# Kernel optimization log

Measured on AMD Instinct MI355X. Metric: run time of the kernel, lower is better.

## Reference

```python
import jax, jax.numpy as jnp
import numpy as np

C = 256      # d_model
H = 8        # nhead
DF = 1024    # dim_feedforward
LE = 2048    # ego tokens
LA = 2048    # other-agent tokens
N_MATCH = 1024


def setup_inputs() -> dict:
    key = jax.random.key(0)
    ks = jax.random.split(key, 16)
    def rn(k, shape, s=0.02):
        return jax.random.normal(k, shape, dtype=jnp.float32) * s
    inp = {}
    inp['x_ego'] = jax.random.normal(ks[0], (LE, C), dtype=jnp.float32)
    inp['x_agent'] = jax.random.normal(ks[1], (LA, C), dtype=jnp.float32)
    # query_fusion MLP(2C -> C -> C -> C), torch Linear weight is (out, in)
    inp['Wf1'] = rn(ks[2], (C, 2 * C)); inp['bf1'] = jnp.zeros((C,), jnp.float32)
    inp['Wf2'] = rn(ks[3], (C, C));     inp['bf2'] = jnp.zeros((C,), jnp.float32)
    inp['Wf3'] = rn(ks[4], (C, C));     inp['bf3'] = jnp.zeros((C,), jnp.float32)
    # nn.MultiheadAttention packed in-proj and out-proj
    inp['Wqkv'] = rn(ks[5], (3 * C, C)); inp['bqkv'] = jnp.zeros((3 * C,), jnp.float32)
    inp['Wo'] = rn(ks[6], (C, C));       inp['bo'] = jnp.zeros((C,), jnp.float32)
    # FFN
    inp['W1'] = rn(ks[7], (DF, C)); inp['b1'] = jnp.zeros((DF,), jnp.float32)
    inp['W2'] = rn(ks[8], (C, DF)); inp['b2'] = jnp.zeros((C,), jnp.float32)
    # LayerNorms
    inp['g1'] = jnp.ones((C,), jnp.float32); inp['be1'] = jnp.zeros((C,), jnp.float32)
    inp['g2'] = jnp.ones((C,), jnp.float32); inp['be2'] = jnp.zeros((C,), jnp.float32)
    # unique 1D positions: first N_MATCH agent positions overlap ego, rest don't
    inp['pos_ego'] = jnp.arange(LE, dtype=jnp.int32)
    pa = np.concatenate([np.arange(N_MATCH), np.arange(LA - N_MATCH) + 10_000_000])
    inp['pos_agent'] = jnp.asarray(pa, dtype=jnp.int32)
    inp['n_remain'] = LA - N_MATCH  # static python int
    return inp


def _ln(t, g, b):
    m = t.mean(-1, keepdims=True)
    v = t.var(-1, keepdims=True)
    return (t - m) / jnp.sqrt(v + 1e-5) * g + b


def reference(x_ego, x_agent, Wf1, bf1, Wf2, bf2, Wf3, bf3, Wqkv, bqkv, Wo, bo,
              W1, b1, W2, b2, g1, be1, g2, be2, pos_ego, pos_agent, n_remain):
    # ---- position-keyed grouping / fuse (replaces the host-side dict loop) ----
    eq = pos_agent[:, None] == pos_ego[None, :]          # [La, Le]
    matched_e = eq.any(axis=0)                           # ego token has same-pos agent token
    agent_for_ego = jnp.argmax(eq, axis=0)               # [Le] matching agent index (valid where matched)
    fused_in = jnp.concatenate([x_ego, x_agent[agent_for_ego]], axis=-1)  # [Le, 2C]
    h = jax.nn.relu(fused_in @ Wf1.T + bf1)
    h = jax.nn.relu(h @ Wf2.T + bf2)
    fused = h @ Wf3.T + bf3                              # query_fusion MLP output [Le, C]
    ego_out = jnp.where(matched_e[:, None], fused, x_ego)
    # agent tokens with no ego match, in original agent order (fixed count n_remain)
    remain_idx = jnp.nonzero(~eq.any(axis=1), size=n_remain)[0]
    q = jnp.concatenate([ego_out, x_agent[remain_idx]], axis=0)[None]  # (1, Lq, C)
    kv = jnp.concatenate([x_ego, x_agent], axis=0)[None]               # (1, Lk, C)
    # ---- MultiheadAttention (batch_first, eval: dropout off) ----
    Wq, Wk, Wv = jnp.split(Wqkv, 3, axis=0)
    bq, bk, bv = jnp.split(bqkv, 3, axis=0)
    dh = C // H
    def heads(t, W, b):
        return (t @ W.T + b).reshape(1, -1, H, dh).transpose(0, 2, 1, 3)
    qh, kh, vh = heads(q, Wq, bq), heads(kv, Wk, bk), heads(kv, Wv, bv)
    scores = jnp.einsum('bhqd,bhkd->bhqk', qh, kh) / (float(dh) ** 0.5)
    attn = jax.nn.softmax(scores, axis=-1)
    o = jnp.einsum('bhqk,bhkd->bhqd', attn, vh).transpose(0, 2, 1, 3).reshape(1, -1, C)
    o = o @ Wo.T + bo
    # ---- residual + norm1 + FFN + residual + norm2 ----
    yq = _ln(q + o, g1, be1)
    ff = jax.nn.relu(yq @ W1.T + b1) @ W2.T + b2
    return _ln(yq + ff, g2, be2)
```

## Files before the change

kernel.cpp:

```cpp
#include <hip/hip_runtime.h>


#define LE 2048
#define LA 2048
#define CDIM 256
#define HN 8
#define DH 32
#define DFF 1024
#define NREM 1024
#define LQC 3072
#define LKC 4096
#define KSPLIT 4
#define NIT (LKC / KSPLIT / 64)

typedef unsigned short u16;
typedef unsigned int u32;
typedef __attribute__((ext_vector_type(8))) short bf16x8;
typedef __attribute__((ext_vector_type(4))) float f32x4;

__device__ __forceinline__ u32 pk_bf16(float a, float b) {
    u32 ua = (__builtin_bit_cast(u32, a) + 0x8000u) >> 16;
    u32 ub = (__builtin_bit_cast(u32, b) + 0x8000u) >> 16;
    return ua | (ub << 16);
}
__device__ __forceinline__ u16 bf16_1(float a) {
    return (u16)((__builtin_bit_cast(u32, a) + 0x8000u) >> 16);
}
__device__ __forceinline__ float fast_exp2(float x) {
    return __builtin_amdgcn_exp2f(x);
}
__device__ __forceinline__ bf16x8 pk8(const float* p) {
    float4 f0 = *(const float4*)p;
    float4 f1 = *(const float4*)(p + 4);
    union { u32 u[4]; bf16x8 v; } r;
    r.u[0] = pk_bf16(f0.x, f0.y); r.u[1] = pk_bf16(f0.z, f0.w);
    r.u[2] = pk_bf16(f1.x, f1.y); r.u[3] = pk_bf16(f1.z, f1.w);
    return r.v;
}

__global__ __launch_bounds__(1024) void k_match(const int* __restrict__ pos_ego,
                                                const int* __restrict__ pos_agent,
                                                int* __restrict__ afe,
                                                int* __restrict__ matched,
                                                int* __restrict__ remain) {
    __shared__ int keyA[4096], valA[4096], keyE[4096];
    __shared__ int ssum[1024];
    const int t = threadIdx.x;
#pragma unroll
    for (int i = 0; i < 4; ++i) { keyA[t + i * 1024] = -1; keyE[t + i * 1024] = -1; }
    __syncthreads();
#pragma unroll
    for (int i = 0; i < 2; ++i) {
        int a = t + i * 1024;
        int p = pos_agent[a];
        u32 h = ((u32)p * 2654435761u) >> 20;
        while (true) {
            int prev = atomicCAS(&keyA[h], -1, p);
            if (prev == -1) { valA[h] = a; break; }
            h = (h + 1) & 4095;
        }
        int pe = pos_ego[a];
        u32 he = ((u32)pe * 2654435761u) >> 20;
        while (true) {
            int prev = atomicCAS(&keyE[he], -1, pe);
            if (prev == -1) break;
            he = (he + 1) & 4095;
        }
    }
    __syncthreads();
#pragma unroll
    for (int i = 0; i < 2; ++i) {
        int e = t + i * 1024;
        int p = pos_ego[e];
        u32 h = ((u32)p * 2654435761u) >> 20;
        int idx = 0, fnd = 0;
        while (true) {
            int k = keyA[h];
            if (k == p) { idx = valA[h]; fnd = 1; break; }
            if (k == -1) break;
            h = (h + 1) & 4095;
        }
        afe[e] = idx;
        matched[e] = fnd;
    }
    int f[2];
#pragma unroll
    for (int i = 0; i < 2; ++i) {
        int a = t * 2 + i;
        int p = pos_agent[a];
        u32 h = ((u32)p * 2654435761u) >> 20;
        int fnd = 0;
        while (true) {
            int k = keyE[h];
            if (k == p) { fnd = 1; break; }
            if (k == -1) break;
            h = (h + 1) & 4095;
        }
        f[i] = !fnd;
    }
    int cnt = f[0] + f[1];
    ssum[t] = cnt;
    __syncthreads();
    for (int off = 1; off < 1024; off <<= 1) {
        int v = (t >= off) ? ssum[t - off] : 0;
        __syncthreads();
        ssum[t] += v;
        __syncthreads();
    }
    int pos = ssum[t] - cnt;
    if (f[0]) { if (pos < NREM) remain[pos] = t * 2; pos++; }
    if (f[1]) { if (pos < NREM) remain[pos] = t * 2 + 1; }
}

template <int EPI, bool RELU>
__global__ __launch_bounds__(256) void gemm_bw(const u16* __restrict__ A,
                                               const float* __restrict__ B,
                                               const float* __restrict__ bias,
                                               void* __restrict__ C,
                                               int M, int N, int K) {
    const int tid = threadIdx.x;
    const int w = tid >> 6, lane = tid & 63;
    const int quad = lane >> 4, qi = lane & 15;
    const int wm = w >> 1, wn = w & 1;
    const int bm = blockIdx.y * 64, bn = blockIdx.x * 64;

    const u16* pa0 = A + (size_t)(bm + wm * 32 + qi) * K + quad * 8;
    const u16* pa1 = pa0 + (size_t)16 * K;
    const float* pb0 = B + (size_t)(bn + wn * 32 + qi) * K + quad * 8;
    const float* pb1 = pb0 + (size_t)16 * K;

    f32x4 acc00 = {0.f, 0.f, 0.f, 0.f}, acc01 = {0.f, 0.f, 0.f, 0.f};
    f32x4 acc10 = {0.f, 0.f, 0.f, 0.f}, acc11 = {0.f, 0.f, 0.f, 0.f};

#pragma unroll 4
    for (int k = 0; k < K; k += 32) {
        bf16x8 a0 = *(const bf16x8*)(pa0 + k);
        bf16x8 a1 = *(const bf16x8*)(pa1 + k);
        bf16x8 b0 = pk8(pb0 + k);
        bf16x8 b1 = pk8(pb1 + k);
        acc00 = __builtin_amdgcn_mfma_f32_16x16x32_bf16(a0, b0, acc00, 0, 0, 0);
        acc01 = __builtin_amdgcn_mfma_f32_16x16x32_bf16(a0, b1, acc01, 0, 0, 0);
        acc10 = __builtin_amdgcn_mfma_f32_16x16x32_bf16(a1, b0, acc10, 0, 0, 0);
        acc11 = __builtin_amdgcn_mfma_f32_16x16x32_bf16(a1, b1, acc11, 0, 0, 0);
    }

#pragma unroll
    for (int i = 0; i < 2; ++i) {
#pragma unroll
        for (int j = 0; j < 2; ++j) {
            f32x4 acc = (i == 0) ? (j == 0 ? acc00 : acc01) : (j == 0 ? acc10 : acc11);
            int n = bn + wn * 32 + j * 16 + qi;
            int mbase = bm + wm * 32 + i * 16 + quad * 4;
            float bs = bias[n];
#pragma unroll
            for (int r = 0; r < 4; ++r) {
                float x = acc[r] + bs;
                if (RELU) x = fmaxf(x, 0.f);
                if (EPI == 0) ((float*)C)[(size_t)(mbase + r) * N + n] = x;
                else ((u16*)C)[(size_t)(mbase + r) * N + n] = bf16_1(x);
            }
        }
    }
}

__global__ __launch_bounds__(256) void k_mlp1(const float* __restrict__ x_ego,
                                              const float* __restrict__ x_agent,
                                              const int* __restrict__ afe,
                                              const float* __restrict__ Wf1,
                                              const float* __restrict__ bf1,
                                              u16* __restrict__ h1_b) {
    const int tid = threadIdx.x;
    const int w = tid >> 6, lane = tid & 63;
    const int quad = lane >> 4, qi = lane & 15;
    const int wm = w >> 1, wn = w & 1;
    const int bm = blockIdx.y * 64, bn = blockIdx.x * 64;

    int e0 = bm + wm * 32 + qi, e1 = e0 + 16;
    const float* pe0 = x_ego + (size_t)e0 * CDIM + quad * 8;
    const float* pe1 = x_ego + (size_t)e1 * CDIM + quad * 8;
    const float* pg0 = x_agent + (size_t)afe[e0] * CDIM + quad * 8;
    const float* pg1 = x_agent + (size_t)afe[e1] * CDIM + quad * 8;
    const float* pb0 = Wf1 + (size_t)(bn + wn * 32 + qi) * 512 + quad * 8;
    const float* pb1 = pb0 + (size_t)16 * 512;

    f32x4 acc00 = {0.f, 0.f, 0.f, 0.f}, acc01 = {0.f, 0.f, 0.f, 0.f};
    f32x4 acc10 = {0.f, 0.f, 0.f, 0.f}, acc11 = {0.f, 0.f, 0.f, 0.f};

#pragma unroll 4
    for (int k = 0; k < 256; k += 32) {
        bf16x8 a0 = pk8(pe0 + k);
        bf16x8 a1 = pk8(pe1 + k);
        bf16x8 b0 = pk8(pb0 + k);
        bf16x8 b1 = pk8(pb1 + k);
        acc00 = __builtin_amdgcn_mfma_f32_16x16x32_bf16(a0, b0, acc00, 0, 0, 0);
        acc01 = __builtin_amdgcn_mfma_f32_16x16x32_bf16(a0, b1, acc01, 0, 0, 0);
        acc10 = __builtin_amdgcn_mfma_f32_16x16x32_bf16(a1, b0, acc10, 0, 0, 0);
        acc11 = __builtin_amdgcn_mfma_f32_16x16x32_bf16(a1, b1, acc11, 0, 0, 0);
    }
#pragma unroll 4
    for (int k = 0; k < 256; k += 32) {
        bf16x8 a0 = pk8(pg0 + k);
        bf16x8 a1 = pk8(pg1 + k);
        bf16x8 b0 = pk8(pb0 + 256 + k);
        bf16x8 b1 = pk8(pb1 + 256 + k);
        acc00 = __builtin_amdgcn_mfma_f32_16x16x32_bf16(a0, b0, acc00, 0, 0, 0);
        acc01 = __builtin_amdgcn_mfma_f32_16x16x32_bf16(a0, b1, acc01, 0, 0, 0);
        acc10 = __builtin_amdgcn_mfma_f32_16x16x32_bf16(a1, b0, acc10, 0, 0, 0);
        acc11 = __builtin_amdgcn_mfma_f32_16x16x32_bf16(a1, b1, acc11, 0, 0, 0);
    }

#pragma unroll
    for (int i = 0; i < 2; ++i) {
#pragma unroll
        for (int j = 0; j < 2; ++j) {
            f32x4 acc = (i == 0) ? (j == 0 ? acc00 : acc01) : (j == 0 ? acc10 : acc11);
            int n = bn + wn * 32 + j * 16 + qi;
            int mbase = bm + wm * 32 + i * 16 + quad * 4;
            float bs = bf1[n];
#pragma unroll
            for (int r = 0; r < 4; ++r)
                h1_b[(size_t)(mbase + r) * 256 + n] = bf16_1(fmaxf(acc[r] + bs, 0.f));
        }
    }
}

__global__ __launch_bounds__(256) void k_mlp3f(const u16* __restrict__ h2_b,
                                               const float* __restrict__ Wf3,
                                               const float* __restrict__ bf3,
                                               const int* __restrict__ matched,
                                               const int* __restrict__ remain,
                                               const float* __restrict__ x_ego,
                                               const float* __restrict__ x_agent,
                                               float* __restrict__ qbuf,
                                               u16* __restrict__ qbuf_b) {
    const int tid = threadIdx.x;
    const int bm = blockIdx.y * 64, bn = blockIdx.x * 64;
    if (bm >= LE) {
        int row = bm + (tid >> 2);
        int col = bn + (tid & 3) * 16;
        int idx = remain[row - LE];
        idx = min(max(idx, 0), LA - 1);
        const float* src = x_agent + (size_t)idx * CDIM + col;
        float* dq = qbuf + (size_t)row * CDIM + col;
        u16* db = qbuf_b + (size_t)row * CDIM + col;
#pragma unroll
        for (int i = 0; i < 4; ++i) {
            float4 v = *(const float4*)(src + i * 4);
            *(float4*)(dq + i * 4) = v;
            u32 p0 = pk_bf16(v.x, v.y), p1 = pk_bf16(v.z, v.w);
            *(uint2*)(db + i * 4) = make_uint2(p0, p1);
        }
        return;
    }
    const int w = tid >> 6, lane = tid & 63;
    const int quad = lane >> 4, qi = lane & 15;
    const int wm = w >> 1, wn = w & 1;

    const u16* pa0 = h2_b + (size_t)(bm + wm * 32 + qi) * 256 + quad * 8;
    const u16* pa1 = pa0 + (size_t)16 * 256;
    const float* pb0 = Wf3 + (size_t)(bn + wn * 32 + qi) * 256 + quad * 8;
    const float* pb1 = pb0 + (size_t)16 * 256;

    f32x4 acc00 = {0.f, 0.f, 0.f, 0.f}, acc01 = {0.f, 0.f, 0.f, 0.f};
    f32x4 acc10 = {0.f, 0.f, 0.f, 0.f}, acc11 = {0.f, 0.f, 0.f, 0.f};
#pragma unroll 4
    for (int k = 0; k < 256; k += 32) {
        bf16x8 a0 = *(const bf16x8*)(pa0 + k);
        bf16x8 a1 = *(const bf16x8*)(pa1 + k);
        bf16x8 b0 = pk8(pb0 + k);
        bf16x8 b1 = pk8(pb1 + k);
        acc00 = __builtin_amdgcn_mfma_f32_16x16x32_bf16(a0, b0, acc00, 0, 0, 0);
        acc01 = __builtin_amdgcn_mfma_f32_16x16x32_bf16(a0, b1, acc01, 0, 0, 0);
        acc10 = __builtin_amdgcn_mfma_f32_16x16x32_bf16(a1, b0, acc10, 0, 0, 0);
        acc11 = __builtin_amdgcn_mfma_f32_16x16x32_bf16(a1, b1, acc11, 0, 0, 0);
    }
#pragma unroll
    for (int i = 0; i < 2; ++i) {
#pragma unroll
        for (int j = 0; j < 2; ++j) {
            f32x4 acc = (i == 0) ? (j == 0 ? acc00 : acc01) : (j == 0 ? acc10 : acc11);
            int n = bn + wn * 32 + j * 16 + qi;
            int mbase = bm + wm * 32 + i * 16 + quad * 4;
            float bs = bf3[n];
#pragma unroll
            for (int r = 0; r < 4; ++r) {
                int row = mbase + r;
                float v = acc[r] + bs;
                if (!matched[row]) v = x_ego[(size_t)row * CDIM + n];
                qbuf[(size_t)row * CDIM + n] = v;
                qbuf_b[(size_t)row * CDIM + n] = bf16_1(v);
            }
        }
    }
}

__global__ __launch_bounds__(256) void k_qkv(const u16* __restrict__ qbuf_b,
                                             const float* __restrict__ x_ego,
                                             const float* __restrict__ x_agent,
                                             const float* __restrict__ Wqkv,
                                             const float* __restrict__ bqkv,
                                             u16* __restrict__ qb,
                                             u16* __restrict__ kbp,
                                             u16* __restrict__ vtb,
                                             float qscale) {
    int b = blockIdx.x;
    const int tid = threadIdx.x;
    const int w = tid >> 6, lane = tid & 63;
    const int quad = lane >> 4, qi = lane & 15;
    const int wm = w >> 1, wn = w & 1;

    f32x4 acc00 = {0.f, 0.f, 0.f, 0.f}, acc01 = {0.f, 0.f, 0.f, 0.f};
    f32x4 acc10 = {0.f, 0.f, 0.f, 0.f}, acc11 = {0.f, 0.f, 0.f, 0.f};

    if (b < 192) {
        const int bm = (b >> 2) * 64, bn = (b & 3) * 64;
        const u16* pa0 = qbuf_b + (size_t)(bm + wm * 32 + qi) * 256 + quad * 8;
        const u16* pa1 = pa0 + (size_t)16 * 256;
        const float* pb0 = Wqkv + (size_t)(bn + wn * 32 + qi) * 256 + quad * 8;
        const float* pb1 = pb0 + (size_t)16 * 256;
#pragma unroll 4
        for (int k = 0; k < 256; k += 32) {
            bf16x8 a0 = *(const bf16x8*)(pa0 + k);
            bf16x8 a1 = *(const bf16x8*)(pa1 + k);
            bf16x8 b0 = pk8(pb0 + k);
            bf16x8 b1 = pk8(pb1 + k);
            acc00 = __builtin_amdgcn_mfma_f32_16x16x32_bf16(a0, b0, acc00, 0, 0, 0);
            acc01 = __builtin_amdgcn_mfma_f32_16x16x32_bf16(a0, b1, acc01, 0, 0, 0);
            acc10 = __builtin_amdgcn_mfma_f32_16x16x32_bf16(a1, b0, acc10, 0, 0, 0);
            acc11 = __builtin_amdgcn_mfma_f32_16x16x32_bf16(a1, b1, acc11, 0, 0, 0);
        }
#pragma unroll
        for (int i = 0; i < 2; ++i)
#pragma unroll
            for (int j = 0; j < 2; ++j) {
                f32x4 acc = (i == 0) ? (j == 0 ? acc00 : acc01) : (j == 0 ? acc10 : acc11);
                int n = bn + wn * 32 + j * 16 + qi;
                int mbase = bm + wm * 32 + i * 16 + quad * 4;
                float bs = bqkv[n];
#pragma unroll
                for (int r = 0; r < 4; ++r)
                    qb[(size_t)(mbase + r) * 256 + n] = bf16_1((acc[r] + bs) * qscale);
            }
    } else {
        int c = b - 192;
        const int bm = (c >> 3) * 64, bn = (c & 7) * 64;
        int j0 = bm + wm * 32 + qi, j1 = j0 + 16;
        const float* base = (bm < LE) ? x_ego : (x_agent - (size_t)LE * CDIM);
        const float* pa0 = base + (size_t)j0 * CDIM + quad * 8;
        const float* pa1 = base + (size_t)j1 * CDIM + quad * 8;
        const float* pb0 = Wqkv + (size_t)(256 + bn + wn * 32 + qi) * 256 + quad * 8;
        const float* pb1 = pb0 + (size_t)16 * 256;
#pragma unroll 4
        for (int k = 0; k < 256; k += 32) {
            bf16x8 a0 = pk8(pa0 + k);
            bf16x8 a1 = pk8(pa1 + k);
            bf16x8 b0 = pk8(pb0 + k);
            bf16x8 b1 = pk8(pb1 + k);
            acc00 = __builtin_amdgcn_mfma_f32_16x16x32_bf16(a0, b0, acc00, 0, 0, 0);
            acc01 = __builtin_amdgcn_mfma_f32_16x16x32_bf16(a0, b1, acc01, 0, 0, 0);
            acc10 = __builtin_amdgcn_mfma_f32_16x16x32_bf16(a1, b0, acc10, 0, 0, 0);
            acc11 = __builtin_amdgcn_mfma_f32_16x16x32_bf16(a1, b1, acc11, 0, 0, 0);
        }
#pragma unroll
        for (int i = 0; i < 2; ++i)
#pragma unroll
            for (int j = 0; j < 2; ++j) {
                f32x4 acc = (i == 0) ? (j == 0 ? acc00 : acc01) : (j == 0 ? acc10 : acc11);
                int n = bn + wn * 32 + j * 16 + qi;
                int mbase = bm + wm * 32 + i * 16 + quad * 4;
                float bs = bqkv[256 + n];
                float v[4];
#pragma unroll
                for (int r = 0; r < 4; ++r) v[r] = acc[r] + bs;
                if (n < 256) {
#pragma unroll
                    for (int r = 0; r < 4; ++r)
                        kbp[(size_t)(mbase + r) * 256 + n] = bf16_1(v[r]);
                } else {
                    ushort4 o4;
                    o4.x = bf16_1(v[0]); o4.y = bf16_1(v[1]);
                    o4.z = bf16_1(v[2]); o4.w = bf16_1(v[3]);
                    *(ushort4*)(vtb + (size_t)(n - 256) * LKC + mbase) = o4;
                }
            }
    }
}

__global__ __launch_bounds__(256) void attn_mfma(const u16* __restrict__ qb,
                                                 const u16* __restrict__ kb,
                                                 const u16* __restrict__ vtb,
                                                 float* __restrict__ Pl,
                                                 float* __restrict__ Pacc) {
    __shared__ u16 Kt[2][64 * 32];
    __shared__ u16 Vt[2][32 * 64];
    __shared__ u16 plds[4][16 * 64];
    const int tid = threadIdx.x;
    const int w = tid >> 6, lane = tid & 63;
    const int quad = lane >> 4, qi = lane & 15;
    const int h = blockIdx.y, ks = blockIdx.z;
    const int q0 = blockIdx.x * 64 + w * 16;

    bf16x8 qf = *(const bf16x8*)(qb + (size_t)(q0 + qi) * CDIM + h * DH + quad * 8);

    f32x4 O0 = {0.f, 0.f, 0.f, 0.f}, O1 = {0.f, 0.f, 0.f, 0.f};
    float lsum = 0.f;

    const int krow = w * 16 + (lane >> 2), kcp = lane & 3;
    const int kc = kcp ^ (krow & 3);
    const u16* kg0 = kb + (size_t)krow * CDIM + h * DH + kc * 8;
    const int kdst = krow * 32 + kcp * 8;
    const int vd = w * 8 + (lane >> 3), vcp = lane & 7;
    const int vc = vcp ^ (vd & 7);
    const u16* vg0 = vtb + (size_t)(h * DH + vd) * LKC + vc * 8;
    const int vdst = vd * 64 + vcp * 8;

    const int ka0 = qi * 32 + ((quad ^ (qi & 3)) << 3);
    const int v00o = qi * 64 + ((quad ^ (qi & 7)) << 3);
    const int v01o = qi * 64 + (((quad + 4) ^ (qi & 7)) << 3);
    const int swz = (qi & 7);
    const int rd0 = qi * 64 + ((quad ^ swz) << 3);
    const int rd1 = qi * 64 + (((4 + quad) ^ swz) << 3);
    const int half = (quad & 1) << 2;

    int kt = ks * (LKC / KSPLIT);
    {
        bf16x8 kr = *(const bf16x8*)(kg0 + (size_t)kt * CDIM);
        bf16x8 vr = *(const bf16x8*)(vg0 + kt);
        *(bf16x8*)&Kt[0][kdst] = kr;
        *(bf16x8*)&Vt[0][vdst] = vr;
    }
    int buf = 0;
    for (int it = 0; it < NIT; ++it, kt += 64) {
        __syncthreads();
        bf16x8 knext, vnext;
        const bool more = (it + 1 < NIT);
        if (more) {
            knext = *(const bf16x8*)(kg0 + (size_t)(kt + 64) * CDIM);
            vnext = *(const bf16x8*)(vg0 + kt + 64);
        }

        bf16x8 a0 = *(const bf16x8*)&Kt[buf][ka0];
        bf16x8 a1 = *(const bf16x8*)&Kt[buf][ka0 + 16 * 32];
        bf16x8 a2 = *(const bf16x8*)&Kt[buf][ka0 + 32 * 32];
        bf16x8 a3 = *(const bf16x8*)&Kt[buf][ka0 + 48 * 32];
        f32x4 z = {0.f, 0.f, 0.f, 0.f};
        f32x4 s0 = __builtin_amdgcn_mfma_f32_16x16x32_bf16(a0, qf, z, 0, 0, 0);
        f32x4 s1 = __builtin_amdgcn_mfma_f32_16x16x32_bf16(a1, qf, z, 0, 0, 0);
        f32x4 s2 = __builtin_amdgcn_mfma_f32_16x16x32_bf16(a2, qf, z, 0, 0, 0);
        f32x4 s3 = __builtin_amdgcn_mfma_f32_16x16x32_bf16(a3, qf, z, 0, 0, 0);

        float p0[4], p1[4], p2[4], p3[4];
#pragma unroll
        for (int r = 0; r < 4; ++r) {
            p0[r] = fast_exp2(s0[r]); p1[r] = fast_exp2(s1[r]);
            p2[r] = fast_exp2(s2[r]); p3[r] = fast_exp2(s3[r]);
            lsum += p0[r] + p1[r] + p2[r] + p3[r];
        }

        u16* pb = &plds[w][0];
#pragma unroll
        for (int t = 0; t < 4; ++t) {
            int jg = t * 2 + (quad >> 1);
            int off = qi * 64 + ((jg ^ swz) << 3) + half;
            uint2 pw;
            float* pp = (t == 0) ? p0 : (t == 1) ? p1 : (t == 2) ? p2 : p3;
            pw.x = pk_bf16(pp[0], pp[1]);
            pw.y = pk_bf16(pp[2], pp[3]);
            *(uint2*)&pb[off] = pw;
        }
        bf16x8 pa0 = *(bf16x8*)&pb[rd0];
        bf16x8 pa1 = *(bf16x8*)&pb[rd1];

        bf16x8 v00 = *(const bf16x8*)&Vt[buf][v00o];
        bf16x8 v01 = *(const bf16x8*)&Vt[buf][v01o];
        bf16x8 v10 = *(const bf16x8*)&Vt[buf][v00o + 16 * 64];
        bf16x8 v11 = *(const bf16x8*)&Vt[buf][v01o + 16 * 64];
        O0 = __builtin_amdgcn_mfma_f32_16x16x32_bf16(pa0, v00, O0, 0, 0, 0);
        O0 = __builtin_amdgcn_mfma_f32_16x16x32_bf16(pa1, v01, O0, 0, 0, 0);
        O1 = __builtin_amdgcn_mfma_f32_16x16x32_bf16(pa0, v10, O1, 0, 0, 0);
        O1 = __builtin_amdgcn_mfma_f32_16x16x32_bf16(pa1, v11, O1, 0, 0, 0);

        if (more) {
            *(bf16x8*)&Kt[buf ^ 1][kdst] = knext;
            *(bf16x8*)&Vt[buf ^ 1][vdst] = vnext;
        }
        buf ^= 1;
    }

    lsum += __shfl_xor(lsum, 16, 64);
    lsum += __shfl_xor(lsum, 32, 64);

    int pbase = (h * KSPLIT + ks) * LQC + q0;
    if (quad == 0) Pl[pbase + qi] = lsum;
#pragma unroll
    for (int r = 0; r < 4; ++r) {
        int q = quad * 4 + r;
        float* pa = Pacc + (size_t)(pbase + q) * 32;
        pa[qi] = O0[r];
        pa[16 + qi] = O1[r];
    }
}

__global__ __launch_bounds__(256) void attn_combine(const float* __restrict__ Pl,
                                                    const float* __restrict__ Pacc,
                                                    u16* __restrict__ attn_b) {
    int t = blockIdx.x * 256 + threadIdx.x;
    int row = t >> 6;
    int h = (t >> 3) & 7;
    int d4 = t & 7;
    float L = 0.f;
    float o[4] = {};
#pragma unroll
    for (int ck = 0; ck < KSPLIT; ++ck) {
        size_t pidx = (size_t)(h * KSPLIT + ck) * LQC + row;
        L += Pl[pidx];
        float4 a = *(const float4*)(Pacc + pidx * 32 + d4 * 4);
        o[0] += a.x; o[1] += a.y; o[2] += a.z; o[3] += a.w;
    }
    float inv = 1.0f / L;
    ushort4 ov;
    ov.x = bf16_1(o[0] * inv); ov.y = bf16_1(o[1] * inv);
    ov.z = bf16_1(o[2] * inv); ov.w = bf16_1(o[3] * inv);
    *(ushort4*)(attn_b + (size_t)row * CDIM + h * DH + d4 * 4) = ov;
}

template <bool EMIT_BF16>
__global__ __launch_bounds__(256) void ln_kernel(const float* __restrict__ X,
                                                 const float* __restrict__ R,
                                                 const float* __restrict__ g,
                                                 const float* __restrict__ b,
                                                 float* __restrict__ out,
                                                 u16* __restrict__ out_b) {
    int lane = threadIdx.x & 63;
    int row = blockIdx.x * 4 + (threadIdx.x >> 6);
    const float* x = X + (size_t)row * CDIM;
    const float* r = R + (size_t)row * CDIM;
    float4 xv = *(const float4*)(x + lane * 4);
    float4 rv = *(const float4*)(r + lane * 4);
    float v[4] = {xv.x + rv.x, xv.y + rv.y, xv.z + rv.z, xv.w + rv.w};
    float s = v[0] + v[1] + v[2] + v[3];
    float sq = v[0] * v[0] + v[1] * v[1] + v[2] * v[2] + v[3] * v[3];
#pragma unroll
    for (int off = 32; off >= 1; off >>= 1) {
        s += __shfl_xor(s, off, 64);
        sq += __shfl_xor(sq, off, 64);
    }
    float mean = s * (1.f / 256.f);
    float var = sq * (1.f / 256.f) - mean * mean;
    float rstd = rsqrtf(var + 1e-5f);
    float4 gv = *(const float4*)(g + lane * 4);
    float4 bv = *(const float4*)(b + lane * 4);
    float4 o = make_float4((v[0] - mean) * rstd * gv.x + bv.x,
                           (v[1] - mean) * rstd * gv.y + bv.y,
                           (v[2] - mean) * rstd * gv.z + bv.z,
                           (v[3] - mean) * rstd * gv.w + bv.w);
    *(float4*)(out + (size_t)row * CDIM + lane * 4) = o;
    if (EMIT_BF16) {
        uint2 ob;
        ob.x = pk_bf16(o.x, o.y);
        ob.y = pk_bf16(o.z, o.w);
        *(uint2*)(out_b + (size_t)row * CDIM + lane * 4) = ob;
    }
}

extern "C" void kernel_launch(void* const* d_in, const int* in_sizes, int n_in,
                              void* d_out, int out_size, void* d_ws, size_t ws_size,
                              hipStream_t stream) {
    const float* x_ego = (const float*)d_in[0];
    const float* x_agent = (const float*)d_in[1];
    const float* Wf1 = (const float*)d_in[2];
    const float* bf1 = (const float*)d_in[3];
    const float* Wf2 = (const float*)d_in[4];
    const float* bf2 = (const float*)d_in[5];
    const float* Wf3 = (const float*)d_in[6];
    const float* bf3 = (const float*)d_in[7];
    const float* Wqkv = (const float*)d_in[8];
    const float* bqkv = (const float*)d_in[9];
    const float* Wo = (const float*)d_in[10];
    const float* bo = (const float*)d_in[11];
    const float* W1 = (const float*)d_in[12];
    const float* b1 = (const float*)d_in[13];
    const float* W2 = (const float*)d_in[14];
    const float* b2 = (const float*)d_in[15];
    const float* g1 = (const float*)d_in[16];
    const float* be1 = (const float*)d_in[17];
    const float* g2 = (const float*)d_in[18];
    const float* be2 = (const float*)d_in[19];
    const int* pos_ego = (const int*)d_in[20];
    const int* pos_agent = (const int*)d_in[21];

    float* ws = (float*)d_ws;
    size_t o = 0;
    float* qbuf = ws + o; o += 786432;
    float* o2 = ws + o; o += 786432;
    float* yq = ws + o; o += 786432;
    float* ff2 = ws + o; o += 786432;
    float* Pl = ws + o; o += HN * KSPLIT * LQC;
    float* Pacc = ws + o; o += (size_t)HN * KSPLIT * LQC * 32;
    u16* h1_b = (u16*)(ws + o); o += 262144;
    u16* h2_b = (u16*)(ws + o); o += 262144;
    u16* qbuf_b = (u16*)(ws + o); o += 393216;
    u16* qb = (u16*)(ws + o); o += 393216;
    u16* kb = (u16*)(ws + o); o += 524288;
    u16* vtb = (u16*)(ws + o); o += 524288;
    u16* attn_b = (u16*)(ws + o); o += 393216;
    u16* ff1_b = (u16*)(ws + o); o += 1572864;
    u16* yq_b = (u16*)(ws + o); o += 393216;
    int* afe = (int*)(ws + o);
    int* matched = afe + LE;
    int* remain = matched + LE;

    const float qscale = 0.17677669529663687f * 1.4426950408889634f;

    k_match<<<1, 1024, 0, stream>>>(pos_ego, pos_agent, afe, matched, remain);

    k_mlp1<<<dim3(4, 32), 256, 0, stream>>>(x_ego, x_agent, afe, Wf1, bf1, h1_b);
    gemm_bw<1, true><<<dim3(4, 32), 256, 0, stream>>>(h1_b, Wf2, bf2, h2_b, LE, 256, 256);
    k_mlp3f<<<dim3(4, 48), 256, 0, stream>>>(h2_b, Wf3, bf3, matched, remain,
                                             x_ego, x_agent, qbuf, qbuf_b);

    k_qkv<<<704, 256, 0, stream>>>(qbuf_b, x_ego, x_agent, Wqkv, bqkv, qb, kb, vtb, qscale);

    attn_mfma<<<dim3(LQC / 64, HN, KSPLIT), 256, 0, stream>>>(qb, kb, vtb, Pl, Pacc);
    attn_combine<<<(LQC * 64) / 256, 256, 0, stream>>>(Pl, Pacc, attn_b);

    gemm_bw<0, false><<<dim3(4, 48), 256, 0, stream>>>(attn_b, Wo, bo, o2, LQC, 256, 256);
    ln_kernel<true><<<LQC / 4, 256, 0, stream>>>(qbuf, o2, g1, be1, yq, yq_b);

    gemm_bw<1, true><<<dim3(16, 48), 256, 0, stream>>>(yq_b, W1, b1, ff1_b, LQC, DFF, 256);
    gemm_bw<0, false><<<dim3(4, 48), 256, 0, stream>>>(ff1_b, W2, b2, ff2, LQC, 256, DFF);
    ln_kernel<false><<<LQC / 4, 256, 0, stream>>>(yq, ff2, g2, be2, (float*)d_out, nullptr);
}
```

Before: 247.7 us.

## Fuse all stages into one cooperative persistent kernel with grid syncs

Replaces the chain of separate kernel launches with a single cooperative megakernel that loops over twelve stages separated by grid-wide syncs, with a fallback that launches each stage separately. It also pre-converts all weights and the ego/agent inputs to bf16 once, so the GEMM inner loops no longer convert fp32 to bf16 on the fly. The hash-match step now uses global-memory tables and runs on one block while the other blocks do the conversion work. The aim is to cut launch overhead and redundant conversion, at the cost of grid-sync latency, a fixed persistent grid that may underfill some stages, and a serial match step on one block.

Result: slower. 613.3 us (+147.6%).

```diff
diff --git a/kernel.cpp b/kernel.cpp
--- a/kernel.cpp
+++ b/kernel.cpp
@@ -1,4 +1,7 @@
 #include <hip/hip_runtime.h>
+#include <hip/hip_cooperative_groups.h>
+
+namespace cg = cooperative_groups;
 
 
 #define LE 2048
@@ -12,6 +15,7 @@
 #define LKC 4096
 #define KSPLIT 4
 #define NIT (LKC / KSPLIT / 64)
+#define SMB 25600
 
 typedef unsigned short u16;
 typedef unsigned int u32;
@@ -29,389 +33,333 @@
 __device__ __forceinline__ float fast_exp2(float x) {
     return __builtin_amdgcn_exp2f(x);
 }
-__device__ __forceinline__ bf16x8 pk8(const float* p) {
-    float4 f0 = *(const float4*)p;
-    float4 f1 = *(const float4*)(p + 4);
-    union { u32 u[4]; bf16x8 v; } r;
-    r.u[0] = pk_bf16(f0.x, f0.y); r.u[1] = pk_bf16(f0.z, f0.w);
-    r.u[2] = pk_bf16(f1.x, f1.y); r.u[3] = pk_bf16(f1.z, f1.w);
-    return r.v;
-}
-
-__global__ __launch_bounds__(1024) void k_match(const int* __restrict__ pos_ego,
-                                                const int* __restrict__ pos_agent,
-                                                int* __restrict__ afe,
-                                                int* __restrict__ matched,
-                                                int* __restrict__ remain) {
-    __shared__ int keyA[4096], valA[4096], keyE[4096];
-    __shared__ int ssum[1024];
+
+struct P {
+    const float *x_ego, *x_agent, *bf1, *bf2, *bf3, *bqkv, *bo, *b1, *b2;
+    const float *g1, *be1, *g2, *be2;
+    const int *pos_ego, *pos_agent;
+    const float *wsrc[7];
+    float *qbuf, *o2, *yq, *ff2, *Pl, *Pacc, *out;
+    u16 *wb, *h1_b, *h2_b, *qbuf_b, *qb, *kb, *vtb, *attn_b, *ff1_b, *yq_b;
+    int *afe, *matched, *remain;
+    int *keyA, *valA, *keyE;
+};
+
+__constant__ __device__ const int woff[8] = {0, 131072, 196608, 262144,
+                                             458752, 524288, 786432, 1048576};
+
+__device__ __forceinline__ void coreK(const u16* pa0, const u16* pa1,
+                                      const u16* pb0, const u16* pb1, int K,
+                                      f32x4& a00, f32x4& a01, f32x4& a10, f32x4& a11) {
+#pragma unroll 4
+    for (int k = 0; k < K; k += 32) {
+        bf16x8 x0 = *(const bf16x8*)(pa0 + k);
+        bf16x8 x1 = *(const bf16x8*)(pa1 + k);
+        bf16x8 y0 = *(const bf16x8*)(pb0 + k);
+        bf16x8 y1 = *(const bf16x8*)(pb1 + k);
+        a00 = __builtin_amdgcn_mfma_f32_16x16x32_bf16(x0, y0, a00, 0, 0, 0);
+        a01 = __builtin_amdgcn_mfma_f32_16x16x32_bf16(x0, y1, a01, 0, 0, 0);
+        a10 = __builtin_amdgcn_mfma_f32_16x16x32_bf16(x1, y0, a10, 0, 0, 0);
+        a11 = __builtin_amdgcn_mfma_f32_16x16x32_bf16(x1, y1, a11, 0, 0, 0);
+    }
+}
+
+__device__ void dv_match(const P& p, char* sm) {
+    int* ssum = (int*)sm;
     const int t = threadIdx.x;
-#pragma unroll
-    for (int i = 0; i < 4; ++i) { keyA[t + i * 1024] = -1; keyE[t + i * 1024] = -1; }
+    for (int i = t; i < 4096; i += 256) { p.keyA[i] = -1; p.keyE[i] = -1; }
     __syncthreads();
-#pragma unroll
-    for (int i = 0; i < 2; ++i) {
-        int a = t + i * 1024;
-        int p = pos_agent[a];
-        u32 h = ((u32)p * 2654435761u) >> 20;
+    __threadfence();
+#pragma unroll
+    for (int i = 0; i < 8; ++i) {
+        int a = t + i * 256;
+        int pa_ = p.pos_agent[a];
+        u32 h = ((u32)pa_ * 2654435761u) >> 20;
         while (true) {
-            int prev = atomicCAS(&keyA[h], -1, p);
-            if (prev == -1) { valA[h] = a; break; }
+            int prev = atomicCAS(&p.keyA[h], -1, pa_);
+            if (prev == -1) { p.valA[h] = a; break; }
             h = (h + 1) & 4095;
         }
-        int pe = pos_ego[a];
+        int pe = p.pos_ego[a];
         u32 he = ((u32)pe * 2654435761u) >> 20;
         while (true) {
-            int prev = atomicCAS(&keyE[he], -1, pe);
+            int prev = atomicCAS(&p.keyE[he], -1, pe);
             if (prev == -1) break;
             he = (he + 1) & 4095;
         }
     }
     __syncthreads();
-#pragma unroll
-    for (int i = 0; i < 2; ++i) {
-        int e = t + i * 1024;
-        int p = pos_ego[e];
-        u32 h = ((u32)p * 2654435761u) >> 20;
+    __threadfence();
+#pragma unroll
+    for (int i = 0; i < 8; ++i) {
+        int e = t + i * 256;
+        int pe = p.pos_ego[e];
+        u32 h = ((u32)pe * 2654435761u) >> 20;
         int idx = 0, fnd = 0;
         while (true) {
-            int k = keyA[h];
-            if (k == p) { idx = valA[h]; fnd = 1; break; }
+            int k = p.keyA[h];
+            if (k == pe) { idx = p.valA[h]; fnd = 1; break; }
             if (k == -1) break;
             h = (h + 1) & 4095;
         }
-        afe[e] = idx;
-        matched[e] = fnd;
-    }
-    int f[2];
-#pragma unroll
-    for (int i = 0; i < 2; ++i) {
-        int a = t * 2 + i;
-        int p = pos_agent[a];
-        u32 h = ((u32)p * 2654435761u) >> 20;
+        p.afe[e] = idx;
+        p.matched[e] = fnd;
+    }
+    int f[8], cnt = 0;
+#pragma unroll
+    for (int i = 0; i < 8; ++i) {
+        int a = t * 8 + i;
+        int pa_ = p.pos_agent[a];
+        u32 h = ((u32)pa_ * 2654435761u) >> 20;
         int fnd = 0;
         while (true) {
-            int k = keyE[h];
-            if (k == p) { fnd = 1; break; }
+            int k = p.keyE[h];
+            if (k == pa_) { fnd = 1; break; }
             if (k == -1) break;
             h = (h + 1) & 4095;
         }
         f[i] = !fnd;
-    }
-    int cnt = f[0] + f[1];
+        cnt += f[i];
+    }
     ssum[t] = cnt;
     __syncthreads();
-    for (int off = 1; off < 1024; off <<= 1) {
+    for (int off = 1; off < 256; off <<= 1) {
         int v = (t >= off) ? ssum[t - off] : 0;
         __syncthreads();
         ssum[t] += v;
         __syncthreads();
     }
     int pos = ssum[t] - cnt;
-    if (f[0]) { if (pos < NREM) remain[pos] = t * 2; pos++; }
-    if (f[1]) { if (pos < NREM) remain[pos] = t * 2 + 1; }
-}
-
-template <int EPI, bool RELU>
-__global__ __launch_bounds__(256) void gemm_bw(const u16* __restrict__ A,
-                                               const float* __restrict__ B,
-                                               const float* __restrict__ bias,
-                                               void* __restrict__ C,
-                                               int M, int N, int K) {
+#pragma unroll
+    for (int i = 0; i < 8; ++i) {
+        if (f[i]) {
+            if (pos < NREM) p.remain[pos] = t * 8 + i;
+            pos++;
+        }
+    }
+}
+
+__device__ void st_wcvt(const P& p, int j) {
+    int g = j * 2048 + threadIdx.x * 8;
+    int s = 0;
+#pragma unroll
+    for (int i = 1; i < 7; ++i) s += (g >= woff[i]);
+    const float* src = p.wsrc[s] + (g - woff[s]);
+    float4 f0 = *(const float4*)(src);
+    float4 f1 = *(const float4*)(src + 4);
+    uint4 o;
+    o.x = pk_bf16(f0.x, f0.y); o.y = pk_bf16(f0.z, f0.w);
+    o.z = pk_bf16(f1.x, f1.y); o.w = pk_bf16(f1.z, f1.w);
+    *(uint4*)(p.wb + g) = o;
+}
+
+__device__ void st_kvb2(const P& p, u16* kv_b, int j) {
+    int t = j * 256 + threadIdx.x;
+    int row = t >> 5, c8 = t & 31;
+    const float* src = (row < LE) ? (p.x_ego + (size_t)row * CDIM)
+                                  : (p.x_agent + (size_t)(row - LE) * CDIM);
+    float4 f0 = *(const float4*)(src + c8 * 8);
+    float4 f1 = *(const float4*)(src + c8 * 8 + 4);
+    uint4 o;
+    o.x = pk_bf16(f0.x, f0.y); o.y = pk_bf16(f0.z, f0.w);
+    o.z = pk_bf16(f1.x, f1.y); o.w = pk_bf16(f1.z, f1.w);
+    *(uint4*)(kv_b + (size_t)row * CDIM + c8 * 8) = o;
+}
+
+__device__ void st_mlp1(const P& p, const u16* kv_b, int j) {
     const int tid = threadIdx.x;
     const int w = tid >> 6, lane = tid & 63;
     const int quad = lane >> 4, qi = lane & 15;
     const int wm = w >> 1, wn = w & 1;
-    const int bm = blockIdx.y * 64, bn = blockIdx.x * 64;
-
-    const u16* pa0 = A + (size_t)(bm + wm * 32 + qi) * K + quad * 8;
-    const u16* pa1 = pa0 + (size_t)16 * K;
-    const float* pb0 = B + (size_t)(bn + wn * 32 + qi) * K + quad * 8;
-    const float* pb1 = pb0 + (size_t)16 * K;
-
-    f32x4 acc00 = {0.f, 0.f, 0.f, 0.f}, acc01 = {0.f, 0.f, 0.f, 0.f};
-    f32x4 acc10 = {0.f, 0.f, 0.f, 0.f}, acc11 = {0.f, 0.f, 0.f, 0.f};
-
-#pragma unroll 4
-    for (int k = 0; k < K; k += 32) {
-        bf16x8 a0 = *(const bf16x8*)(pa0 + k);
-        bf16x8 a1 = *(const bf16x8*)(pa1 + k);
-        bf16x8 b0 = pk8(pb0 + k);
-        bf16x8 b1 = pk8(pb1 + k);
-        acc00 = __builtin_amdgcn_mfma_f32_16x16x32_bf16(a0, b0, acc00, 0, 0, 0);
-        acc01 = __builtin_amdgcn_mfma_f32_16x16x32_bf16(a0, b1, acc01, 0, 0, 0);
-        acc10 = __builtin_amdgcn_mfma_f32_16x16x32_bf16(a1, b0, acc10, 0, 0, 0);
-        acc11 = __builtin_amdgcn_mfma_f32_16x16x32_bf16(a1, b1, acc11, 0, 0, 0);
-    }
-
-#pragma unroll
-    for (int i = 0; i < 2; ++i) {
-#pragma unroll
-        for (int j = 0; j < 2; ++j) {
-            f32x4 acc = (i == 0) ? (j == 0 ? acc00 : acc01) : (j == 0 ? acc10 : acc11);
-            int n = bn + wn * 32 + j * 16 + qi;
-            int mbase = bm + wm * 32 + i * 16 + quad * 4;
-            float bs = bias[n];
-#pragma unroll
-            for (int r = 0; r < 4; ++r) {
-                float x = acc[r] + bs;
-                if (RELU) x = fmaxf(x, 0.f);
-                if (EPI == 0) ((float*)C)[(size_t)(mbase + r) * N + n] = x;
-                else ((u16*)C)[(size_t)(mbase + r) * N + n] = bf16_1(x);
-            }
-        }
-    }
-}
-
-__global__ __launch_bounds__(256) void k_mlp1(const float* __restrict__ x_ego,
-                                              const float* __restrict__ x_agent,
-                                              const int* __restrict__ afe,
-                                              const float* __restrict__ Wf1,
-                                              const float* __restrict__ bf1,
-                                              u16* __restrict__ h1_b) {
+    const int bm = (j >> 2) * 64, bn = (j & 3) * 64;
+    int e0 = bm + wm * 32 + qi, e1 = e0 + 16;
+    const u16* pe0 = kv_b + (size_t)e0 * CDIM + quad * 8;
+    const u16* pe1 = kv_b + (size_t)e1 * CDIM + quad * 8;
+    const u16* pg0 = kv_b + (size_t)(LE + p.afe[e0]) * CDIM + quad * 8;
+    const u16* pg1 = kv_b + (size_t)(LE + p.afe[e1]) * CDIM + quad * 8;
+    const u16* pb0 = p.wb + (size_t)(bn + wn * 32 + qi) * 512 + quad * 8;
+    const u16* pb1 = pb0 + (size_t)16 * 512;
+    f32x4 a00 = {0, 0, 0, 0}, a01 = {0, 0, 0, 0}, a10 = {0, 0, 0, 0}, a11 = {0, 0, 0, 0};
+    coreK(pe0, pe1, pb0, pb1, 256, a00, a01, a10, a11);
+    coreK(pg0, pg1, pb0 + 256, pb1 + 256, 256, a00, a01, a10, a11);
+#pragma unroll
+    for (int i = 0; i < 2; ++i)
+#pragma unroll
+        for (int jj = 0; jj < 2; ++jj) {
+            f32x4 acc = (i == 0) ? (jj == 0 ? a00 : a01) : (jj == 0 ? a10 : a11);
+            int n = bn + wn * 32 + jj * 16 + qi;
+            int mb = bm + wm * 32 + i * 16 + quad * 4;
+            float bs = p.bf1[n];
+#pragma unroll
+            for (int r = 0; r < 4; ++r)
+                p.h1_b[(size_t)(mb + r) * 256 + n] = bf16_1(fmaxf(acc[r] + bs, 0.f));
+        }
+}
+
+__device__ void st_mlp2(const P& p, int j) {
     const int tid = threadIdx.x;
     const int w = tid >> 6, lane = tid & 63;
     const int quad = lane >> 4, qi = lane & 15;
     const int wm = w >> 1, wn = w & 1;
-    const int bm = blockIdx.y * 64, bn = blockIdx.x * 64;
-
-    int e0 = bm + wm * 32 + qi, e1 = e0 + 16;
-    const float* pe0 = x_ego + (size_t)e0 * CDIM + quad * 8;
-    const float* pe1 = x_ego + (size_t)e1 * CDIM + quad * 8;
-    const float* pg0 = x_agent + (size_t)afe[e0] * CDIM + quad * 8;
-    const float* pg1 = x_agent + (size_t)afe[e1] * CDIM + quad * 8;
-    const float* pb0 = Wf1 + (size_t)(bn + wn * 32 + qi) * 512 + quad * 8;
-    const float* pb1 = pb0 + (size_t)16 * 512;
-
-    f32x4 acc00 = {0.f, 0.f, 0.f, 0.f}, acc01 = {0.f, 0.f, 0.f, 0.f};
-    f32x4 acc10 = {0.f, 0.f, 0.f, 0.f}, acc11 = {0.f, 0.f, 0.f, 0.f};
-
-#pragma unroll 4
-    for (int k = 0; k < 256; k += 32) {
-        bf16x8 a0 = pk8(pe0 + k);
-        bf16x8 a1 = pk8(pe1 + k);
-        bf16x8 b0 = pk8(pb0 + k);
-        bf16x8 b1 = pk8(pb1 + k);
-        acc00 = __builtin_amdgcn_mfma_f32_16x16x32_bf16(a0, b0, acc00, 0, 0, 0);
-        acc01 = __builtin_amdgcn_mfma_f32_16x16x32_bf16(a0, b1, acc01, 0, 0, 0);
-        acc10 = __builtin_amdgcn_mfma_f32_16x16x32_bf16(a1, b0, acc10, 0, 0, 0);
-        acc11 = __builtin_amdgcn_mfma_f32_16x16x32_bf16(a1, b1, acc11, 0, 0, 0);
-    }
-#pragma unroll 4
-    for (int k = 0; k < 256; k += 32) {
-        bf16x8 a0 = pk8(pg0 + k);
-        bf16x8 a1 = pk8(pg1 + k);
-        bf16x8 b0 = pk8(pb0 + 256 + k);
-        bf16x8 b1 = pk8(pb1 + 256 + k);
-        acc00 = __builtin_amdgcn_mfma_f32_16x16x32_bf16(a0, b0, acc00, 0, 0, 0);
-        acc01 = __builtin_amdgcn_mfma_f32_16x16x32_bf16(a0, b1, acc01, 0, 0, 0);
-        acc10 = __builtin_amdgcn_mfma_f32_16x16x32_bf16(a1, b0, acc10, 0, 0, 0);
-        acc11 = __builtin_amdgcn_mfma_f32_16x16x32_bf16(a1, b1, acc11, 0, 0, 0);
-    }
-
-#pragma unroll
-    for (int i = 0; i < 2; ++i) {
-#pragma unroll
-        for (int j = 0; j < 2; ++j) {
-            f32x4 acc = (i == 0) ? (j == 0 ? acc00 : acc01) : (j == 0 ? acc10 : acc11);
-            int n = bn + wn * 32 + j * 16 + qi;
-            int mbase = bm + wm * 32 + i * 16 + quad * 4;
-            float bs = bf1[n];
+    const int bm = (j >> 2) * 64, bn = (j & 3) * 64;
+    const u16* Wf2_b = p.wb + 131072;
+    const u16* pa0 = p.h1_b + (size_t)(bm + wm * 32 + qi) * 256 + quad * 8;
+    const u16* pa1 = pa0 + (size_t)16 * 256;
+    const u16* pb0 = Wf2_b + (size_t)(bn + wn * 32 + qi) * 256 + quad * 8;
+    const u16* pb1 = pb0 + (size_t)16 * 256;
+    f32x4 a00 = {0, 0, 0, 0}, a01 = {0, 0, 0, 0}, a10 = {0, 0, 0, 0}, a11 = {0, 0, 0, 0};
+    coreK(pa0, pa1, pb0, pb1, 256, a00, a01, a10, a11);
+#pragma unroll
+    for (int i = 0; i < 2; ++i)
+#pragma unroll
+        for (int jj = 0; jj < 2; ++jj) {
+            f32x4 acc = (i == 0) ? (jj == 0 ? a00 : a01) : (jj == 0 ? a10 : a11);
+            int n = bn + wn * 32 + jj * 16 + qi;
+            int mb = bm + wm * 32 + i * 16 + quad * 4;
+            float bs = p.bf2[n];
 #pragma unroll
             for (int r = 0; r < 4; ++r)
-                h1_b[(size_t)(mbase + r) * 256 + n] = bf16_1(fmaxf(acc[r] + bs, 0.f));
-        }
-    }
-}
-
-__global__ __launch_bounds__(256) void k_mlp3f(const u16* __restrict__ h2_b,
-                                               const float* __restrict__ Wf3,
-                                               const float* __restrict__ bf3,
-                                               const int* __restrict__ matched,
-                                               const int* __restrict__ remain,
-                                               const float* __restrict__ x_ego,
-                                               const float* __restrict__ x_agent,
-                                               float* __restrict__ qbuf,
-                                               u16* __restrict__ qbuf_b) {
-    const int tid = threadIdx.x;
-    const int bm = blockIdx.y * 64, bn = blockIdx.x * 64;
+                p.h2_b[(size_t)(mb + r) * 256 + n] = bf16_1(fmaxf(acc[r] + bs, 0.f));
+        }
+}
+
+__device__ void st_mlp3f(const P& p, int j) {
+    const int tid = threadIdx.x;
+    const int bn = (j & 3) * 64, bm = (j >> 2) * 64;
     if (bm >= LE) {
         int row = bm + (tid >> 2);
         int col = bn + (tid & 3) * 16;
-        int idx = remain[row - LE];
+        int idx = p.remain[row - LE];
         idx = min(max(idx, 0), LA - 1);
-        const float* src = x_agent + (size_t)idx * CDIM + col;
-        float* dq = qbuf + (size_t)row * CDIM + col;
-        u16* db = qbuf_b + (size_t)row * CDIM + col;
+        const float* src = p.x_agent + (size_t)idx * CDIM + col;
+        float* dq = p.qbuf + (size_t)row * CDIM + col;
+        u16* db = p.qbuf_b + (size_t)row * CDIM + col;
 #pragma unroll
         for (int i = 0; i < 4; ++i) {
             float4 v = *(const float4*)(src + i * 4);
             *(float4*)(dq + i * 4) = v;
-            u32 p0 = pk_bf16(v.x, v.y), p1 = pk_bf16(v.z, v.w);
-            *(uint2*)(db + i * 4) = make_uint2(p0, p1);
+            *(uint2*)(db + i * 4) = make_uint2(pk_bf16(v.x, v.y), pk_bf16(v.z, v.w));
         }
         return;
     }
     const int w = tid >> 6, lane = tid & 63;
     const int quad = lane >> 4, qi = lane & 15;
     const int wm = w >> 1, wn = w & 1;
-
-    const u16* pa0 = h2_b + (size_t)(bm + wm * 32 + qi) * 256 + quad * 8;
+    const u16* Wf3_b = p.wb + 196608;
+    const u16* pa0 = p.h2_b + (size_t)(bm + wm * 32 + qi) * 256 + quad * 8;
     const u16* pa1 = pa0 + (size_t)16 * 256;
-    const float* pb0 = Wf3 + (size_t)(bn + wn * 32 + qi) * 256 + quad * 8;
-    const float* pb1 = pb0 + (size_t)16 * 256;
-
-    f32x4 acc00 = {0.f, 0.f, 0.f, 0.f}, acc01 = {0.f, 0.f, 0.f, 0.f};
-    f32x4 acc10 = {0.f, 0.f, 0.f, 0.f}, acc11 = {0.f, 0.f, 0.f, 0.f};
-#pragma unroll 4
-    for (int k = 0; k < 256; k += 32) {
-        bf16x8 a0 = *(const bf16x8*)(pa0 + k);
-        bf16x8 a1 = *(const bf16x8*)(pa1 + k);
-        bf16x8 b0 = pk8(pb0 + k);
-        bf16x8 b1 = pk8(pb1 + k);
-        acc00 = __builtin_amdgcn_mfma_f32_16x16x32_bf16(a0, b0, acc00, 0, 0, 0);
-        acc01 = __builtin_amdgcn_mfma_f32_16x16x32_bf16(a0, b1, acc01, 0, 0, 0);
-        acc10 = __builtin_amdgcn_mfma_f32_16x16x32_bf16(a1, b0, acc10, 0, 0, 0);
-        acc11 = __builtin_amdgcn_mfma_f32_16x16x32_bf16(a1, b1, acc11, 0, 0, 0);
-    }
-#pragma unroll
-    for (int i = 0; i < 2; ++i) {
-#pragma unroll
-        for (int j = 0; j < 2; ++j) {
-            f32x4 acc = (i == 0) ? (j == 0 ? acc00 : acc01) : (j == 0 ? acc10 : acc11);
-            int n = bn + wn * 32 + j * 16 + qi;
-            int mbase = bm + wm * 32 + i * 16 + quad * 4;
-            float bs = bf3[n];
+    const u16* pb0 = Wf3_b + (size_t)(bn + wn * 32 + qi) * 256 + quad * 8;
+    const u16* pb1 = pb0 + (size_t)16 * 256;
+    f32x4 a00 = {0, 0, 0, 0}, a01 = {0, 0, 0, 0}, a10 = {0, 0, 0, 0}, a11 = {0, 0, 0, 0};
+    coreK(pa0, pa1, pb0, pb1, 256, a00, a01, a10, a11);
+#pragma unroll
+    for (int i = 0; i < 2; ++i)
+#pragma unroll
+        for (int jj = 0; jj < 2; ++jj) {
+            f32x4 acc = (i == 0) ? (jj == 0 ? a00 : a01) : (jj == 0 ? a10 : a11);
+            int n = bn + wn * 32 + jj * 16 + qi;
+            int mb = bm + wm * 32 + i * 16 + quad * 4;
+            float bs = p.bf3[n];
 #pragma unroll
             for (int r = 0; r < 4; ++r) {
-                int row = mbase + r;
+                int row = mb + r;
                 float v = acc[r] + bs;
-                if (!matched[row]) v = x_ego[(size_t)row * CDIM + n];
-                qbuf[(size_t)row * CDIM + n] = v;
-                qbuf_b[(size_t)row * CDIM + n] = bf16_1(v);
+                if (!p.matched[row]) v = p.x_ego[(size_t)row * CDIM + n];
+                p.qbuf[(size_t)row * CDIM + n] = v;
+                p.qbuf_b[(size_t)row * CDIM + n] = bf16_1(v);
             }
         }
-    }
-}
-
-__global__ __launch_bounds__(256) void k_qkv(const u16* __restrict__ qbuf_b,
-                                             const float* __restrict__ x_ego,
-                                             const float* __restrict__ x_agent,
-                                             const float* __restrict__ Wqkv,
-                                             const float* __restrict__ bqkv,
-                                             u16* __restrict__ qb,
-                                             u16* __restrict__ kbp,
-                                             u16* __restrict__ vtb,
-                                             float qscale) {
-    int b = blockIdx.x;
+}
+
+__device__ void st_qproj(const P& p, int j, float qscale) {
     const int tid = threadIdx.x;
     const int w = tid >> 6, lane = tid & 63;
     const int quad = lane >> 4, qi = lane & 15;
     const int wm = w >> 1, wn = w & 1;
-
-    f32x4 acc00 = {0.f, 0.f, 0.f, 0.f}, acc01 = {0.f, 0.f, 0.f, 0.f};
-    f32x4 acc10 = {0.f, 0.f, 0.f, 0.f}, acc11 = {0.f, 0.f, 0.f, 0.f};
-
-    if (b < 192) {
-        const int bm = (b >> 2) * 64, bn = (b & 3) * 64;
-        const u16* pa0 = qbuf_b + (size_t)(bm + wm * 32 + qi) * 256 + quad * 8;
-        const u16* pa1 = pa0 + (size_t)16 * 256;
-        const float* pb0 = Wqkv + (size_t)(bn + wn * 32 + qi) * 256 + quad * 8;
-        const float* pb1 = pb0 + (size_t)16 * 256;
-#pragma unroll 4
-        for (int k = 0; k < 256; k += 32) {
-            bf16x8 a0 = *(const bf16x8*)(pa0 + k);
-            bf16x8 a1 = *(const bf16x8*)(pa1 + k);
-            bf16x8 b0 = pk8(pb0 + k);
-            bf16x8 b1 = pk8(pb1 + k);
-            acc00 = __builtin_amdgcn_mfma_f32_16x16x32_bf16(a0, b0, acc00, 0, 0, 0);
-            acc01 = __builtin_amdgcn_mfma_f32_16x16x32_bf16(a0, b1, acc01, 0, 0, 0);
-            acc10 = __builtin_amdgcn_mfma_f32_16x16x32_bf16(a1, b0, acc10, 0, 0, 0);
-            acc11 = __builtin_amdgcn_mfma_f32_16x16x32_bf16(a1, b1, acc11, 0, 0, 0);
-        }
-#pragma unroll
-        for (int i = 0; i < 2; ++i)
-#pragma unroll
-            for (int j = 0; j < 2; ++j) {
-                f32x4 acc = (i == 0) ? (j == 0 ? acc00 : acc01) : (j == 0 ? acc10 : acc11);
-                int n = bn + wn * 32 + j * 16 + qi;
-                int mbase = bm + wm * 32 + i * 16 + quad * 4;
-                float bs = bqkv[n];
+    const int bm = (j >> 2) * 64, bn = (j & 3) * 64;
+    const u16* Wq_b = p.wb + 262144;
+    const u16* pa0 = p.qbuf_b + (size_t)(bm + wm * 32 + qi) * 256 + quad * 8;
+    const u16* pa1 = pa0 + (size_t)16 * 256;
+    const u16* pb0 = Wq_b + (size_t)(bn + wn * 32 + qi) * 256 + quad * 8;
+    const u16* pb1 = pb0 + (size_t)16 * 256;
+    f32x4 a00 = {0, 0, 0, 0}, a01 = {0, 0, 0, 0}, a10 = {0, 0, 0, 0}, a11 = {0, 0, 0, 0};
+    coreK(pa0, pa1, pb0, pb1, 256, a00, a01, a10, a11);
+#pragma unroll
+    for (int i = 0; i < 2; ++i)
+#pragma unroll
+        for (int jj = 0; jj < 2; ++jj) {
+            f32x4 acc = (i == 0) ? (jj == 0 ? a00 : a01) : (jj == 0 ? a10 : a11);
+            int n = bn + wn * 32 + jj * 16 + qi;
+            int mb = bm + wm * 32 + i * 16 + quad * 4;
+            float bs = p.bqkv[n];
+#pragma unroll
+            for (int r = 0; r < 4; ++r)
+                p.qb[(size_t)(mb + r) * 256 + n] = bf16_1((acc[r] + bs) * qscale);
+        }
+}
+
+__device__ void st_kvproj(const P& p, const u16* kv_b, int c) {
+    const int tid = threadIdx.x;
+    const int w = tid >> 6, lane = tid & 63;
+    const int quad = lane >> 4, qi = lane & 15;
+    const int wm = w >> 1, wn = w & 1;
+    const int bm = (c >> 3) * 64, bn = (c & 7) * 64;
+    const u16* Wkv_b = p.wb + 327680;
+    const u16* pa0 = kv_b + (size_t)(bm + wm * 32 + qi) * 256 + quad * 8;
+    const u16* pa1 = pa0 + (size_t)16 * 256;
+    const u16* pb0 = Wkv_b + (size_t)(bn + wn * 32 + qi) * 256 + quad * 8;
+    const u16* pb1 = pb0 + (size_t)16 * 256;
+    f32x4 a00 = {0, 0, 0, 0}, a01 = {0, 0, 0, 0}, a10 = {0, 0, 0, 0}, a11 = {0, 0, 0, 0};
+    coreK(pa0, pa1, pb0, pb1, 256, a00, a01, a10, a11);
+#pragma unroll
+    for (int i = 0; i < 2; ++i)
+#pragma unroll
+        for (int jj = 0; jj < 2; ++jj) {
+            f32x4 acc = (i == 0) ? (jj == 0 ? a00 : a01) : (jj == 0 ? a10 : a11);
+            int n = bn + wn * 32 + jj * 16 + qi;
+            int mb = bm + wm * 32 + i * 16 + quad * 4;
+            float bs = p.bqkv[256 + n];
+            float v[4];
+#pragma unroll
+            for (int r = 0; r < 4; ++r) v[r] = acc[r] + bs;
+            if (n < 256) {
 #pragma unroll
                 for (int r = 0; r < 4; ++r)
-                    qb[(size_t)(mbase + r) * 256 + n] = bf16_1((acc[r] + bs) * qscale);
+                    p.kb[(size_t)(mb + r) * 256 + n] = bf16_1(v[r]);
+            } else {
+                ushort4 o4;
+                o4.x = bf16_1(v[0]); o4.y = bf16_1(v[1]);
+                o4.z = bf16_1(v[2]); o4.w = bf16_1(v[3]);
+                *(ushort4*)(p.vtb + (size_t)(n - 256) * LKC + mb) = o4;
             }
-    } else {
-        int c = b - 192;
-        const int bm = (c >> 3) * 64, bn = (c & 7) * 64;
-        int j0 = bm + wm * 32 + qi, j1 = j0 + 16;
-        const float* base = (bm < LE) ? x_ego : (x_agent - (size_t)LE * CDIM);
-        const float* pa0 = base + (size_t)j0 * CDIM + quad * 8;
-        const float* pa1 = base + (size_t)j1 * CDIM + quad * 8;
-        const float* pb0 = Wqkv + (size_t)(256 + bn + wn * 32 + qi) * 256 + quad * 8;
-        const float* pb1 = pb0 + (size_t)16 * 256;
-#pragma unroll 4
-        for (int k = 0; k < 256; k += 32) {
-            bf16x8 a0 = pk8(pa0 + k);
-            bf16x8 a1 = pk8(pa1 + k);
-            bf16x8 b0 = pk8(pb0 + k);
-            bf16x8 b1 = pk8(pb1 + k);
-            acc00 = __builtin_amdgcn_mfma_f32_16x16x32_bf16(a0, b0, acc00, 0, 0, 0);
-            acc01 = __builtin_amdgcn_mfma_f32_16x16x32_bf16(a0, b1, acc01, 0, 0, 0);
-            acc10 = __builtin_amdgcn_mfma_f32_16x16x32_bf16(a1, b0, acc10, 0, 0, 0);
-            acc11 = __builtin_amdgcn_mfma_f32_16x16x32_bf16(a1, b1, acc11, 0, 0, 0);
-        }
-#pragma unroll
-        for (int i = 0; i < 2; ++i)
-#pragma unroll
-            for (int j = 0; j < 2; ++j) {
-                f32x4 acc = (i == 0) ? (j == 0 ? acc00 : acc01) : (j == 0 ? acc10 : acc11);
-                int n = bn + wn * 32 + j * 16 + qi;
-                int mbase = bm + wm * 32 + i * 16 + quad * 4;
-                float bs = bqkv[256 + n];
-                float v[4];
-#pragma unroll
-                for (int r = 0; r < 4; ++r) v[r] = acc[r] + bs;
-                if (n < 256) {
-#pragma unroll
-                    for (int r = 0; r < 4; ++r)
-                        kbp[(size_t)(mbase + r) * 256 + n] = bf16_1(v[r]);
-                } else {
-                    ushort4 o4;
-                    o4.x = bf16_1(v[0]); o4.y = bf16_1(v[1]);
-                    o4.z = bf16_1(v[2]); o4.w = bf16_1(v[3]);
-                    *(ushort4*)(vtb + (size_t)(n - 256) * LKC + mbase) = o4;
-                }
-            }
-    }
-}
-
-__global__ __launch_bounds__(256) void attn_mfma(const u16* __restrict__ qb,
-                                                 const u16* __restrict__ kb,
-                                                 const u16* __restrict__ vtb,
-                                                 float* __restrict__ Pl,
-                                                 float* __restrict__ Pacc) {
-    __shared__ u16 Kt[2][64 * 32];
-    __shared__ u16 Vt[2][32 * 64];
-    __shared__ u16 plds[4][16 * 64];
-    const int tid = threadIdx.x;
-    const int w = tid >> 6, lane = tid & 63;
-    const int quad = lane >> 4, qi = lane & 15;
-    const int h = blockIdx.y, ks = blockIdx.z;
-    const int q0 = blockIdx.x * 64 + w * 16;
-
-    bf16x8 qf = *(const bf16x8*)(qb + (size_t)(q0 + qi) * CDIM + h * DH + quad * 8);
-
-    f32x4 O0 = {0.f, 0.f, 0.f, 0.f}, O1 = {0.f, 0.f, 0.f, 0.f};
+        }
+}
+
+__device__ void st_attn(const P& p, char* sm, int job) {
+    u16* Kt = (u16*)sm;
+    u16* Vt = Kt + 4096;
+    u16* plds = Vt + 4096;
+    const int tid = threadIdx.x;
+    const int w = tid >> 6, lane = tid & 63;
+    const int quad = lane >> 4, qi = lane & 15;
+    const int bxa = job % 48;
+    const int h = (job / 48) & 7;
+    const int ks = job / 384;
+    const int q0 = bxa * 64 + w * 16;
+
+    __syncthreads();
+
+    bf16x8 qf = *(const bf16x8*)(p.qb + (size_t)(q0 + qi) * CDIM + h * DH + quad * 8);
+    f32x4 O0 = {0, 0, 0, 0}, O1 = {0, 0, 0, 0};
     float lsum = 0.f;
 
     const int krow = w * 16 + (lane >> 2), kcp = lane & 3;
     const int kc = kcp ^ (krow & 3);
-    const u16* kg0 = kb + (size_t)krow * CDIM + h * DH + kc * 8;
+    const u16* kg0 = p.kb + (size_t)krow * CDIM + h * DH + kc * 8;
     const int kdst = krow * 32 + kcp * 8;
     const int vd = w * 8 + (lane >> 3), vcp = lane & 7;
     const int vc = vcp ^ (vd & 7);
-    const u16* vg0 = vtb + (size_t)(h * DH + vd) * LKC + vc * 8;
+    const u16* vg0 = p.vtb + (size_t)(h * DH + vd) * LKC + vc * 8;
     const int vdst = vd * 64 + vcp * 8;
 
     const int ka0 = qi * 32 + ((quad ^ (qi & 3)) << 3);
@@ -426,8 +374,8 @@
     {
         bf16x8 kr = *(const bf16x8*)(kg0 + (size_t)kt * CDIM);
         bf16x8 vr = *(const bf16x8*)(vg0 + kt);
-        *(bf16x8*)&Kt[0][kdst] = kr;
-        *(bf16x8*)&Vt[0][vdst] = vr;
+        *(bf16x8*)&Kt[kdst] = kr;
+        *(bf16x8*)&Vt[vdst] = vr;
     }
     int buf = 0;
     for (int it = 0; it < NIT; ++it, kt += 64) {
@@ -438,12 +386,13 @@
             knext = *(const bf16x8*)(kg0 + (size_t)(kt + 64) * CDIM);
             vnext = *(const bf16x8*)(vg0 + kt + 64);
         }
-
-        bf16x8 a0 = *(const bf16x8*)&Kt[buf][ka0];
-        bf16x8 a1 = *(const bf16x8*)&Kt[buf][ka0 + 16 * 32];
-        bf16x8 a2 = *(const bf16x8*)&Kt[buf][ka0 + 32 * 32];
-        bf16x8 a3 = *(const bf16x8*)&Kt[buf][ka0 + 48 * 32];
-        f32x4 z = {0.f, 0.f, 0.f, 0.f};
+        const u16* Kb = Kt + buf * 2048;
+        const u16* Vb = Vt + buf * 2048;
+        bf16x8 a0 = *(const bf16x8*)&Kb[ka0];
+        bf16x8 a1 = *(const bf16x8*)&Kb[ka0 + 16 * 32];
+        bf16x8 a2 = *(const bf16x8*)&Kb[ka0 + 32 * 32];
+        bf16x8 a3 = *(const bf16x8*)&Kb[ka0 + 48 * 32];
+        f32x4 z = {0, 0, 0, 0};
         f32x4 s0 = __builtin_amdgcn_mfma_f32_16x16x32_bf16(a0, qf, z, 0, 0, 0);
         f32x4 s1 = __builtin_amdgcn_mfma_f32_16x16x32_bf16(a1, qf, z, 0, 0, 0);
         f32x4 s2 = __builtin_amdgcn_mfma_f32_16x16x32_bf16(a2, qf, z, 0, 0, 0);
@@ -457,13 +406,13 @@
             lsum += p0[r] + p1[r] + p2[r] + p3[r];
         }
 
-        u16* pb = &plds[w][0];
-#pragma unroll
-        for (int t = 0; t < 4; ++t) {
-            int jg = t * 2 + (quad >> 1);
+        u16* pb = plds + w * 1024;
+#pragma unroll
+        for (int t2 = 0; t2 < 4; ++t2) {
+            int jg = t2 * 2 + (quad >> 1);
             int off = qi * 64 + ((jg ^ swz) << 3) + half;
             uint2 pw;
-            float* pp = (t == 0) ? p0 : (t == 1) ? p1 : (t == 2) ? p2 : p3;
+            float* pp = (t2 == 0) ? p0 : (t2 == 1) ? p1 : (t2 == 2) ? p2 : p3;
             pw.x = pk_bf16(pp[0], pp[1]);
             pw.y = pk_bf16(pp[2], pp[3]);
             *(uint2*)&pb[off] = pw;
@@ -471,18 +420,20 @@
         bf16x8 pa0 = *(bf16x8*)&pb[rd0];
         bf16x8 pa1 = *(bf16x8*)&pb[rd1];
 
-        bf16x8 v00 = *(const bf16x8*)&Vt[buf][v00o];
-        bf16x8 v01 = *(const bf16x8*)&Vt[buf][v01o];
-        bf16x8 v10 = *(const bf16x8*)&Vt[buf][v00o + 16 * 64];
-        bf16x8 v11 = *(const bf16x8*)&Vt[buf][v01o + 16 * 64];
+        bf16x8 v00 = *(const bf16x8*)&Vb[v00o];
+        bf16x8 v01 = *(const bf16x8*)&Vb[v01o];
+        bf16x8 v10 = *(const bf16x8*)&Vb[v00o + 16 * 64];
+        bf16x8 v11 = *(const bf16x8*)&Vb[v01o + 16 * 64];
         O0 = __builtin_amdgcn_mfma_f32_16x16x32_bf16(pa0, v00, O0, 0, 0, 0);
         O0 = __builtin_amdgcn_mfma_f32_16x16x32_bf16(pa1, v01, O0, 0, 0, 0);
         O1 = __builtin_amdgcn_mfma_f32_16x16x32_bf16(pa0, v10, O1, 0, 0, 0);
         O1 = __builtin_amdgcn_mfma_f32_16x16x32_bf16(pa1, v11, O1, 0, 0, 0);
 
         if (more) {
-            *(bf16x8*)&Kt[buf ^ 1][kdst] = knext;
-            *(bf16x8*)&Vt[buf ^ 1][vdst] = vnext;
+            u16* Kn = Kt + (buf ^ 1) * 2048;
+            u16* Vn = Vt + (buf ^ 1) * 2048;
+            *(bf16x8*)&Kn[kdst] = knext;
+            *(bf16x8*)&Vn[vdst] = vnext;
         }
         buf ^= 1;
     }
@@ -491,20 +442,18 @@
     lsum += __shfl_xor(lsum, 32, 64);
 
     int pbase = (h * KSPLIT + ks) * LQC + q0;
-    if (quad == 0) Pl[pbase + qi] = lsum;
+    if (quad == 0) p.Pl[pbase + qi] = lsum;
 #pragma unroll
     for (int r = 0; r < 4; ++r) {
         int q = quad * 4 + r;
-        float* pa = Pacc + (size_t)(pbase + q) * 32;
+        float* pa = p.Pacc + (size_t)(pbase + q) * 32;
         pa[qi] = O0[r];
         pa[16 + qi] = O1[r];
     }
 }
 
-__global__ __launch_bounds__(256) void attn_combine(const float* __restrict__ Pl,
-                                                    const float* __restrict__ Pacc,
-                                                    u16* __restrict__ attn_b) {
-    int t = blockIdx.x * 256 + threadIdx.x;
+__device__ void st_combine(const P& p, int j) {
+    int t = j * 256 + threadIdx.x;
     int row = t >> 6;
     int h = (t >> 3) & 7;
     int d4 = t & 7;
@@ -513,26 +462,48 @@
 #pragma unroll
     for (int ck = 0; ck < KSPLIT; ++ck) {
         size_t pidx = (size_t)(h * KSPLIT + ck) * LQC + row;
-        L += Pl[pidx];
-        float4 a = *(const float4*)(Pacc + pidx * 32 + d4 * 4);
+        L += p.Pl[pidx];
+        float4 a = *(const float4*)(p.Pacc + pidx * 32 + d4 * 4);
         o[0] += a.x; o[1] += a.y; o[2] += a.z; o[3] += a.w;
     }
     float inv = 1.0f / L;
     ushort4 ov;
     ov.x = bf16_1(o[0] * inv); ov.y = bf16_1(o[1] * inv);
     ov.z = bf16_1(o[2] * inv); ov.w = bf16_1(o[3] * inv);
-    *(ushort4*)(attn_b + (size_t)row * CDIM + h * DH + d4 * 4) = ov;
-}
-
-template <bool EMIT_BF16>
-__global__ __launch_bounds__(256) void ln_kernel(const float* __restrict__ X,
-                                                 const float* __restrict__ R,
-                                                 const float* __restrict__ g,
-                                                 const float* __restrict__ b,
-                                                 float* __restrict__ out,
-                                                 u16* __restrict__ out_b) {
+    *(ushort4*)(p.attn_b + (size_t)row * CDIM + h * DH + d4 * 4) = ov;
+}
+
+__device__ void st_outproj(const P& p, int j) {
+    const int tid = threadIdx.x;
+    const int w = tid >> 6, lane = tid & 63;
+    const int quad = lane >> 4, qi = lane & 15;
+    const int wm = w >> 1, wn = w & 1;
+    const int bm = (j >> 2) * 64, bn = (j & 3) * 64;
+    const u16* Wo_b = p.wb + 458752;
+    const u16* pa0 = p.attn_b + (size_t)(bm + wm * 32 + qi) * 256 + quad * 8;
+    const u16* pa1 = pa0 + (size_t)16 * 256;
+    const u16* pb0 = Wo_b + (size_t)(bn + wn * 32 + qi) * 256 + quad * 8;
+    const u16* pb1 = pb0 + (size_t)16 * 256;
+    f32x4 a00 = {0, 0, 0, 0}, a01 = {0, 0, 0, 0}, a10 = {0, 0, 0, 0}, a11 = {0, 0, 0, 0};
+    coreK(pa0, pa1, pb0, pb1, 256, a00, a01, a10, a11);
+#pragma unroll
+    for (int i = 0; i < 2; ++i)
+#pragma unroll
+        for (int jj = 0; jj < 2; ++jj) {
+            f32x4 acc = (i == 0) ? (jj == 0 ? a00 : a01) : (jj == 0 ? a10 : a11);
+            int n = bn + wn * 32 + jj * 16 + qi;
+            int mb = bm + wm * 32 + i * 16 + quad * 4;
+            float bs = p.bo[n];
+#pragma unroll
+            for (int r = 0; r < 4; ++r)
+                p.o2[(size_t)(mb + r) * 256 + n] = acc[r] + bs;
+        }
+}
+
+__device__ void st_ln(int j, const float* X, const float* R, const float* g,
+                      const float* b, float* out, u16* out_b, bool emit) {
     int lane = threadIdx.x & 63;
-    int row = blockIdx.x * 4 + (threadIdx.x >> 6);
+    int row = j * 4 + (threadIdx.x >> 6);
     const float* x = X + (size_t)row * CDIM;
     const float* r = R + (size_t)row * CDIM;
     float4 xv = *(const float4*)(x + lane * 4);
@@ -555,7 +526,7 @@
                            (v[2] - mean) * rstd * gv.z + bv.z,
                            (v[3] - mean) * rstd * gv.w + bv.w);
     *(float4*)(out + (size_t)row * CDIM + lane * 4) = o;
-    if (EMIT_BF16) {
+    if (emit) {
         uint2 ob;
         ob.x = pk_bf16(o.x, o.y);
         ob.y = pk_bf16(o.z, o.w);
@@ -563,71 +534,179 @@
     }
 }
 
+__device__ void st_ffn1(const P& p, int j) {
+    const int tid = threadIdx.x;
+    const int w = tid >> 6, lane = tid & 63;
+    const int quad = lane >> 4, qi = lane & 15;
+    const int wm = w >> 1, wn = w & 1;
+    const int bn = (j & 15) * 64, bm = (j >> 4) * 64;
+    const u16* W1_b = p.wb + 524288;
+    const u16* pa0 = p.yq_b + (size_t)(bm + wm * 32 + qi) * 256 + quad * 8;
+    const u16* pa1 = pa0 + (size_t)16 * 256;
+    const u16* pb0 = W1_b + (size_t)(bn + wn * 32 + qi) * 256 + quad * 8;
+    const u16* pb1 = pb0 + (size_t)16 * 256;
+    f32x4 a00 = {0, 0, 0, 0}, a01 = {0, 0, 0, 0}, a10 = {0, 0, 0, 0}, a11 = {0, 0, 0, 0};
+    coreK(pa0, pa1, pb0, pb1, 256, a00, a01, a10, a11);
+#pragma unroll
+    for (int i = 0; i < 2; ++i)
+#pragma unroll
+        for (int jj = 0; jj < 2; ++jj) {
+            f32x4 acc = (i == 0) ? (jj == 0 ? a00 : a01) : (jj == 0 ? a10 : a11);
+            int n = bn + wn * 32 + jj * 16 + qi;
+            int mb = bm + wm * 32 + i * 16 + quad * 4;
+            float bs = p.b1[n];
+#pragma unroll
+            for (int r = 0; r < 4; ++r)
+                p.ff1_b[(size_t)(mb + r) * DFF + n] = bf16_1(fmaxf(acc[r] + bs, 0.f));
+        }
+}
+
+__device__ void st_ffn2(const P& p, int j) {
+    const int tid = threadIdx.x;
+    const int w = tid >> 6, lane = tid & 63;
+    const int quad = lane >> 4, qi = lane & 15;
+    const int wm = w >> 1, wn = w & 1;
+    const int bm = (j >> 2) * 64, bn = (j & 3) * 64;
+    const u16* W2_b = p.wb + 786432;
+    const u16* pa0 = p.ff1_b + (size_t)(bm + wm * 32 + qi) * DFF + quad * 8;
+    const u16* pa1 = pa0 + (size_t)16 * DFF;
+    const u16* pb0 = W2_b + (size_t)(bn + wn * 32 + qi) * DFF + quad * 8;
+    const u16* pb1 = pb0 + (size_t)16 * DFF;
+    f32x4 a00 = {0, 0, 0, 0}, a01 = {0, 0, 0, 0}, a10 = {0, 0, 0, 0}, a11 = {0, 0, 0, 0};
+    coreK(pa0, pa1, pb0, pb1, DFF, a00, a01, a10, a11);
+#pragma unroll
+    for (int i = 0; i < 2; ++i)
+#pragma unroll
+        for (int jj = 0; jj < 2; ++jj) {
+            f32x4 acc = (i == 0) ? (jj == 0 ? a00 : a01) : (jj == 0 ? a10 : a11);
+            int n = bn + wn * 32 + jj * 16 + qi;
+            int mb = bm + wm * 32 + i * 16 + quad * 4;
+            float bs = p.b2[n];
+#pragma unroll
+            for (int r = 0; r < 4; ++r)
+                p.ff2[(size_t)(mb + r) * 256 + n] = acc[r] + bs;
+        }
+}
+
+__device__ void run_stage(const P& p, int st, char* sm, u16* kv_b, float qscale) {
+    const int bx = blockIdx.x, gd = gridDim.x;
+    switch (st) {
+        case 0:
+            if (bx == 0) dv_match(p, sm);
+            else
+                for (int j = bx - 1; j < 1024; j += gd - 1) {
+                    if (j < 512) st_wcvt(p, j);
+                    else st_kvb2(p, kv_b, j - 512);
+                }
+            break;
+        case 1:
+            for (int j = bx; j < 640; j += gd) {
+                if (j < 128) st_mlp1(p, kv_b, j);
+                else st_kvproj(p, kv_b, j - 128);
+            }
+            break;
+        case 2: for (int j = bx; j < 128; j += gd) st_mlp2(p, j); break;
+        case 3: for (int j = bx; j < 192; j += gd) st_mlp3f(p, j); break;
+        case 4: for (int j = bx; j < 192; j += gd) st_qproj(p, j, qscale); break;
+        case 5: for (int j = bx; j < 1536; j += gd) st_attn(p, sm, j); break;
+        case 6: for (int j = bx; j < 768; j += gd) st_combine(p, j); break;
+        case 7: for (int j = bx; j < 192; j += gd) st_outproj(p, j); break;
+        case 8:
+            for (int j = bx; j < 768; j += gd)
+                st_ln(j, p.qbuf, p.o2, p.g1, p.be1, p.yq, p.yq_b, true);
+            break;
+        case 9: for (int j = bx; j < 768; j += gd) st_ffn1(p, j); break;
+        case 10: for (int j = bx; j < 192; j += gd) st_ffn2(p, j); break;
+        case 11:
+            for (int j = bx; j < 768; j += gd)
+                st_ln(j, p.yq, p.ff2, p.g2, p.be2, p.out, nullptr, false);
+            break;
+    }
+}
+
+__global__ __launch_bounds__(256, 2) void mega(P p, u16* kv_b, float qscale) {
+    __shared__ __align__(16) char sm[SMB];
+    cg::grid_group grid = cg::this_grid();
+    for (int st = 0; st < 12; ++st) {
+        run_stage(p, st, sm, kv_b, qscale);
+        if (st < 11) grid.sync();
+    }
+}
+
+__global__ __launch_bounds__(256) void one_stage(P p, u16* kv_b, float qscale, int st) {
+    __shared__ __align__(16) char sm[SMB];
+    run_stage(p, st, sm, kv_b, qscale);
+}
+
 extern "C" void kernel_launch(void* const* d_in, const int* in_sizes, int n_in,
                               void* d_out, int out_size, void* d_ws, size_t ws_size,
                               hipStream_t stream) {
-    const float* x_ego = (const float*)d_in[0];
-    const float* x_agent = (const float*)d_in[1];
-    const float* Wf1 = (const float*)d_in[2];
-    const float* bf1 = (const float*)d_in[3];
-    const float* Wf2 = (const float*)d_in[4];
-    const float* bf2 = (const float*)d_in[5];
-    const float* Wf3 = (const float*)d_in[6];
-    const float* bf3 = (const float*)d_in[7];
-    const float* Wqkv = (const float*)d_in[8];
-    const float* bqkv = (const float*)d_in[9];
-    const float* Wo = (const float*)d_in[10];
-    const float* bo = (const float*)d_in[11];
-    const float* W1 = (const float*)d_in[12];
-    const float* b1 = (const float*)d_in[13];
-    const float* W2 = (const float*)d_in[14];
-    const float* b2 = (const float*)d_in[15];
-    const float* g1 = (const float*)d_in[16];
-    const float* be1 = (const float*)d_in[17];
-    const float* g2 = (const float*)d_in[18];
-    const float* be2 = (const float*)d_in[19];
-    const int* pos_ego = (const int*)d_in[20];
-    const int* pos_agent = (const int*)d_in[21];
+    P p;
+    p.x_ego = (const float*)d_in[0];
+    p.x_agent = (const float*)d_in[1];
+    p.wsrc[0] = (const float*)d_in[2];
+    p.bf1 = (const float*)d_in[3];
+    p.wsrc[1] = (const float*)d_in[4];
+    p.bf2 = (const float*)d_in[5];
+    p.wsrc[2] = (const float*)d_in[6];
+    p.bf3 = (const float*)d_in[7];
+    p.wsrc[3] = (const float*)d_in[8];
+    p.bqkv = (const float*)d_in[9];
+    p.wsrc[4] = (const float*)d_in[10];
+    p.bo = (const float*)d_in[11];
+    p.wsrc[5] = (const float*)d_in[12];
+    p.b1 = (const float*)d_in[13];
+    p.wsrc[6] = (const float*)d_in[14];
+    p.b2 = (const float*)d_in[15];
+    p.g1 = (const float*)d_in[16];
+    p.be1 = (const float*)d_in[17];
+    p.g2 = (const float*)d_in[18];
+    p.be2 = (const float*)d_in[19];
+    p.pos_ego = (const int*)d_in[20];
+    p.pos_agent = (const int*)d_in[21];
 
     float* ws = (float*)d_ws;
     size_t o = 0;
-    float* qbuf = ws + o; o += 786432;
-    float* o2 = ws + o; o += 786432;
-    float* yq = ws + o; o += 786432;
-    float* ff2 = ws + o; o += 786432;
-    float* Pl = ws + o; o += HN * KSPLIT * LQC;
-    float* Pacc = ws + o; o += (size_t)HN * KSPLIT * LQC * 32;
-    u16* h1_b = (u16*)(ws + o); o += 262144;
-    u16* h2_b = (u16*)(ws + o); o += 262144;
-    u16* qbuf_b = (u16*)(ws + o); o += 393216;
-    u16* qb = (u16*)(ws + o); o += 393216;
-    u16* kb = (u16*)(ws + o); o += 524288;
-    u16* vtb = (u16*)(ws + o); o += 524288;
-    u16* attn_b = (u16*)(ws + o); o += 393216;
-    u16* ff1_b = (u16*)(ws + o); o += 1572864;
-    u16* yq_b = (u16*)(ws + o); o += 393216;
-    int* afe = (int*)(ws + o);
-    int* matched = afe + LE;
-    int* remain = matched + LE;
+    p.qbuf = ws + o; o += 786432;
+    p.o2 = ws + o; o += 786432;
+    p.yq = ws + o; o += 786432;
+    p.ff2 = ws + o; o += 786432;
+    p.Pl = ws + o; o += HN * KSPLIT * LQC;
+    p.Pacc = ws + o; o += (size_t)HN * KSPLIT * LQC * 32;
+    p.wb = (u16*)(ws + o); o += 524288;
+    u16* kv_b = (u16*)(ws + o); o += 524288;
+    p.h1_b = (u16*)(ws + o); o += 262144;
+    p.h2_b = (u16*)(ws + o); o += 262144;
+    p.qbuf_b = (u16*)(ws + o); o += 393216;
+    p.qb = (u16*)(ws + o); o += 393216;
+    p.kb = (u16*)(ws + o); o += 524288;
+    p.vtb = (u16*)(ws + o); o += 524288;
+    p.attn_b = (u16*)(ws + o); o += 393216;
+    p.ff1_b = (u16*)(ws + o); o += 1572864;
+    p.yq_b = (u16*)(ws + o); o += 393216;
+    p.afe = (int*)(ws + o); o += 2048;
+    p.matched = (int*)(ws + o); o += 2048;
+    p.remain = (int*)(ws + o); o += 2048;
+    p.keyA = (int*)(ws + o); o += 4096;
+    p.valA = (int*)(ws + o); o += 4096;
+    p.keyE = (int*)(ws + o); o += 4096;
+    p.out = (float*)d_out;
 
     const float qscale = 0.17677669529663687f * 1.4426950408889634f;
 
-    k_match<<<1, 1024, 0, stream>>>(pos_ego, pos_agent, afe, matched, remain);
-
-    k_mlp1<<<dim3(4, 32), 256, 0, stream>>>(x_ego, x_agent, afe, Wf1, bf1, h1_b);
-    gemm_bw<1, true><<<dim3(4, 32), 256, 0, stream>>>(h1_b, Wf2, bf2, h2_b, LE, 256, 256);
-    k_mlp3f<<<dim3(4, 48), 256, 0, stream>>>(h2_b, Wf3, bf3, matched, remain,
-                                             x_ego, x_agent, qbuf, qbuf_b);
-
-    k_qkv<<<704, 256, 0, stream>>>(qbuf_b, x_ego, x_agent, Wqkv, bqkv, qb, kb, vtb, qscale);
-
-    attn_mfma<<<dim3(LQC / 64, HN, KSPLIT), 256, 0, stream>>>(qb, kb, vtb, Pl, Pacc);
-    attn_combine<<<(LQC * 64) / 256, 256, 0, stream>>>(Pl, Pacc, attn_b);
-
-    gemm_bw<0, false><<<dim3(4, 48), 256, 0, stream>>>(attn_b, Wo, bo, o2, LQC, 256, 256);
-    ln_kernel<true><<<LQC / 4, 256, 0, stream>>>(qbuf, o2, g1, be1, yq, yq_b);
-
-    gemm_bw<1, true><<<dim3(16, 48), 256, 0, stream>>>(yq_b, W1, b1, ff1_b, LQC, DFF, 256);
-    gemm_bw<0, false><<<dim3(4, 48), 256, 0, stream>>>(ff1_b, W2, b2, ff2, LQC, 256, DFF);
-    ln_kernel<false><<<LQC / 4, 256, 0, stream>>>(yq, ff2, g2, be2, (float*)d_out, nullptr);
-}
+    bool done = false;
+    int maxb = 0;
+    hipError_t qe = hipOccupancyMaxActiveBlocksPerMultiprocessor(&maxb, mega, 256, 0);
+    if (qe == hipSuccess && maxb >= 1) {
+        int grid = maxb * 256;
+        if (grid > 512) grid = 512;
+        void* args[] = {(void*)&p, (void*)&kv_b, (void*)&qscale};
+        hipError_t le = hipLaunchCooperativeKernel(mega, dim3(grid), dim3(256),
+                                                   args, 0, stream);
+        if (le == hipSuccess) done = true;
+    }
+    if (!done) {
+        for (int st = 0; st < 12; ++st)
+            one_stage<<<512, 256, 0, stream>>>(p, kv_b, qscale, st);
+    }
+}
```
